# Kernel tuning notes

Hardware: AMD Instinct MI355X
Metric: run time of the kernel (lower is better)

Reference implementation:

```python
import jax, jax.numpy as jnp
import numpy as np

V = 30000      # vocab_size
D = 300        # t_embed
H = 4          # GATv2 heads
C = 300        # per-head out channels (hidden_dim = t_embed)
HID = 768      # hidden_size
B = 2
T = 800
NEG = 0.2      # GATv2 negative_slope default


def gatv2_layer(x, src, dst, Wl, bl, Wr, br, att, bias):
    """PyG GATv2Conv, eval mode, add_self_loops=True, concat=True.
    x: [N, Fin]; src/dst: [E] (src->dst message flow).
    Wl/Wr: [Fin, H*C]; bl/br: [H*C]; att: [H, C]; bias: [H*C].
    """
    N = x.shape[0]
    xl = (x @ Wl + bl).reshape(N, H, C)   # source transform
    xr = (x @ Wr + br).reshape(N, H, C)   # target transform
    loops = jnp.arange(N)
    s = jnp.concatenate([src, loops])
    d = jnp.concatenate([dst, loops])
    e = jax.nn.leaky_relu(xl[s] + xr[d], NEG)          # [E', H, C]
    logits = jnp.einsum('ehc,hc->eh', e, att)           # [E', H]
    # scatter-softmax over incoming edges per target node
    mx = jax.ops.segment_max(logits, d, num_segments=N)  # [N, H]
    ex = jnp.exp(logits - mx[d])
    den = jax.ops.segment_sum(ex, d, num_segments=N)
    alpha = ex / den[d]                                   # [E', H]
    out = jax.ops.segment_sum(alpha[:, :, None] * xl[s], d, num_segments=N)
    return out.reshape(N, H * C) + bias


def setup_inputs() -> dict:
    key = jax.random.key(0)
    ks = jax.random.split(key, 20)
    sc = 0.05
    inp = {
        'kg_enc_input': jax.random.randint(ks[0], (B, T, 3), 0, V),
        'embeddings': jax.random.normal(ks[1], (V, D), jnp.float32),
        # conv1: GATv2Conv(D, C, heads=H)
        'Wl1': jax.random.normal(ks[2], (D, H * C), jnp.float32) * sc,
        'bl1': jnp.zeros((H * C,), jnp.float32),
        'Wr1': jax.random.normal(ks[3], (D, H * C), jnp.float32) * sc,
        'br1': jnp.zeros((H * C,), jnp.float32),
        'att1': jax.random.normal(ks[4], (H, C), jnp.float32) * sc,
        'bias1': jnp.zeros((H * C,), jnp.float32),
        # conv2: GATv2Conv(4*C, C, heads=H)
        'Wl2': jax.random.normal(ks[5], (H * C, H * C), jnp.float32) * sc,
        'bl2': jnp.zeros((H * C,), jnp.float32),
        'Wr2': jax.random.normal(ks[6], (H * C, H * C), jnp.float32) * sc,
        'br2': jnp.zeros((H * C,), jnp.float32),
        'att2': jax.random.normal(ks[7], (H, C), jnp.float32) * sc,
        'bias2': jnp.zeros((H * C,), jnp.float32),
        # post_mp: Linear(4*C, C) -> Dropout -> Linear(C, D)
        'Wp1': jax.random.normal(ks[8], (H * C, C), jnp.float32) * sc,
        'bp1': jnp.zeros((C,), jnp.float32),
        'Wp2': jax.random.normal(ks[9], (C, D), jnp.float32) * sc,
        'bp2': jnp.zeros((D,), jnp.float32),
        # lii: Linear(3*D, HID, bias=False)
        'Wlii': jax.random.normal(ks[10], (3 * D, HID), jnp.float32) * sc,
    }
    return inp


def reference(kg_enc_input, embeddings, Wl1, bl1, Wr1, br1, att1, bias1,
              Wl2, bl2, Wr2, br2, att2, bias2, Wp1, bp1, Wp2, bp2, Wlii):
    # original GAT.forward detaches x -> no grad to embedding table
    x0 = jax.lax.stop_gradient(embeddings)

    def per_sample(kg):  # kg: [T, 3]
        head, rel, tail = kg[:, 0], kg[:, 1], kg[:, 2]
        # edge_list = cat([[head;rel], [rel;tail]], dim=1)
        src = jnp.concatenate([head, rel])
        dst = jnp.concatenate([rel, tail])
        h = gatv2_layer(x0, src, dst, Wl1, bl1, Wr1, br1, att1, bias1)
        h = jax.nn.relu(h)                 # dropout: eval mode, identity
        h = gatv2_layer(h, src, dst, Wl2, bl2, Wr2, br2, att2, bias2)
        h = jax.nn.relu(h)
        w = (h @ Wp1 + bp1) @ Wp2 + bp2    # post_mp, [V, D]
        # per-triple gather + concat of (h, r, t) node embeddings
        return jnp.concatenate([w[head], w[rel], w[tail]], axis=-1)  # [T, 3D]

    final = jax.vmap(per_sample)(kg_enc_input)   # [B, T, 3D]
    return final @ Wlii                           # [B, T, HID]
```

## Files before the change

kernel.cpp:

```cpp
#include <hip/hip_runtime.h>
#include <hip/hip_bf16.h>

#define V 30000
#define D 300
#define H 4
#define C 300
#define HC 1200
#define B 2
#define T 800
#define E 1600
#define MAXM 2400
#define NEG 0.2f
#define SCAN_CH ((MAXM + 255) / 256)

#define MR 2432
#define KD 320
#define KHC 1216
#define NLR 2432
#define WB_LD 304
#define KF 928
#define FRW 896

typedef __attribute__((ext_vector_type(8))) unsigned short u16x8;
typedef __attribute__((ext_vector_type(8))) short s16x8;
typedef __attribute__((ext_vector_type(4))) float f32x4;

__device__ inline unsigned short f2b(float v) {
    unsigned u = __float_as_uint(v);
    unsigned r = (u + 0x7FFFu + ((u >> 16) & 1u)) >> 16;
    return (unsigned short)r;
}
__device__ inline float b2f(unsigned short u) {
    return __uint_as_float(((unsigned)u) << 16);
}

#define GLOAD_LDS16(g, l) __builtin_amdgcn_global_load_lds( \
    (const __attribute__((address_space(1))) void*)(g), \
    (__attribute__((address_space(3))) void*)(l), 16, 0, 0)


__global__ void k_init(int* map, int* list, int* deg, int* fill, int* mcnt) {
    int i = blockIdx.x * blockDim.x + threadIdx.x;
    if (i < B * V) map[i] = -1;
    if (i < B * MAXM) { list[i] = 0; deg[i] = 0; fill[i] = 0; }
    if (i < B) mcnt[i] = 0;
}

__global__ void k_mark(const int* __restrict__ kg, int* map) {
    int i = blockIdx.x * blockDim.x + threadIdx.x;
    if (i >= B * T * 3) return;
    int b = i / (T * 3);
    map[b * V + kg[i]] = 1;
}

__global__ void k_compact(int* map, int* list, int* mcnt) {
    int b = blockIdx.y;
    int i = blockIdx.x * 256 + threadIdx.x;
    bool pred = (i < V) && (map[b * V + i] == 1);
    unsigned long long m = __ballot(pred);
    int lane = threadIdx.x & 63;
    int wid = threadIdx.x >> 6;
    __shared__ int wcnt[4];
    __shared__ int base;
    if (lane == 0) wcnt[wid] = __popcll(m);
    __syncthreads();
    if (threadIdx.x == 0) {
        int t = 0;
#pragma unroll
        for (int w2 = 0; w2 < 4; ++w2) { int c = wcnt[w2]; wcnt[w2] = t; t += c; }
        base = t ? atomicAdd(&mcnt[b], t) : 0;
    }
    __syncthreads();
    if (pred) {
        int idx = base + wcnt[wid] + __popcll(m & ((1ull << lane) - 1ull));
        map[b * V + i] = idx;
        list[b * MAXM + idx] = i;
    }
}

__global__ void k_edges(const int* __restrict__ kg, const int* __restrict__ map,
                        int* esrc, int* edst, int* deg, int* tric) {
    int i = blockIdx.x * blockDim.x + threadIdx.x;
    if (i >= B * T) return;
    int b = i / T, t = i % T;
    const int* kk = kg + ((long)b * T + t) * 3;
    int hc = map[b * V + kk[0]];
    int rc = map[b * V + kk[1]];
    int tc = map[b * V + kk[2]];
    int eb = b * E;
    esrc[eb + t]     = hc;  edst[eb + t]     = rc;
    esrc[eb + T + t] = rc;  edst[eb + T + t] = tc;
    atomicAdd(&deg[b * MAXM + rc], 1);
    atomicAdd(&deg[b * MAXM + tc], 1);
    int* tr = tric + ((long)b * T + t) * 3;
    tr[0] = hc; tr[1] = rc; tr[2] = tc;
}

__global__ void k_scan(const int* __restrict__ deg, int* __restrict__ off) {
    int b = blockIdx.x;
    deg += b * MAXM; off += b * (MAXM + 1);
    __shared__ int ts[256];
    int t = threadIdx.x;
    int base = t * SCAN_CH;
    int loc[SCAN_CH];
    int sum = 0;
#pragma unroll
    for (int j = 0; j < SCAN_CH; ++j) {
        int v = (base + j < MAXM) ? deg[base + j] : 0;
        sum += v; loc[j] = sum;
    }
    ts[t] = sum; __syncthreads();
    for (int s = 1; s < 256; s <<= 1) {
        int v = (t >= s) ? ts[t - s] : 0;
        __syncthreads();
        ts[t] += v;
        __syncthreads();
    }
    int excl = (t > 0) ? ts[t - 1] : 0;
#pragma unroll
    for (int j = 0; j < SCAN_CH; ++j)
        if (base + j < MAXM) off[base + j + 1] = excl + loc[j];
    if (t == 0) off[0] = 0;
}

__global__ void k_scatter(const int* __restrict__ esrc, const int* __restrict__ edst,
                          const int* __restrict__ off, int* fill, int* csr) {
    int i = blockIdx.x * blockDim.x + threadIdx.x;
    if (i >= B * E) return;
    int b = i / E;
    int d = edst[i];
    int pos = off[b * (MAXM + 1) + d] + atomicAdd(&fill[b * MAXM + d], 1);
    csr[b * E + pos] = esrc[i];
}

__global__ void k_wt_all(const float* __restrict__ Wl1, const float* __restrict__ Wr1,
                         const float* __restrict__ Wl2, const float* __restrict__ Wr2,
                         const float* __restrict__ Wp1, const float* __restrict__ Wp2,
                         const float* __restrict__ Wlii,
                         const float* __restrict__ bl1, const float* __restrict__ br1,
                         const float* __restrict__ bl2, const float* __restrict__ br2,
                         unsigned short* Wlr1t, unsigned short* Wlr2t,
                         unsigned short* Wp1t, unsigned short* Wp2t, unsigned short* Wft,
                         float* blr1, float* blr2) {
    const int KT[7]  = {10, 10, 38, 38, 38, 10, 29};
    const int CUM[9] = {0, 380, 760, 2204, 3648, 4104, 4224, 4920, 4930};
    int bid = blockIdx.x;
    int task = 0;
    while (bid >= CUM[task + 1]) ++task;
    int local = bid - CUM[task];
    if (task == 7) {
        int c = local * 256 + threadIdx.y * 32 + threadIdx.x;
        if (c < NLR) {
            float v1 = 0.f, v2 = 0.f;
            if (c < 1200) { v1 = bl1[c]; v2 = bl2[c]; }
            else if (c >= 1216 && c < 2416) { v1 = br1[c - 1216]; v2 = br2[c - 1216]; }
            blr1[c] = v1; blr2[c] = v2;
        }
        return;
    }
    int kt = local % KT[task], nt = local / KT[task];
    const float* W; unsigned short* Wt; int K, N, Kp;
    switch (task) {
        case 0: W = Wl1;  Wt = Wlr1t;                     K = 300;  N = 1200; Kp = KD;  break;
        case 1: W = Wr1;  Wt = Wlr1t + (long)1216 * KD;   K = 300;  N = 1200; Kp = KD;  break;
        case 2: W = Wl2;  Wt = Wlr2t;                     K = 1200; N = 1200; Kp = KHC; break;
        case 3: W = Wr2;  Wt = Wlr2t + (long)1216 * KHC;  K = 1200; N = 1200; Kp = KHC; break;
        case 4: W = Wp1;  Wt = Wp1t;                      K = 1200; N = 300;  Kp = KHC; break;
        case 5: W = Wp2;  Wt = Wp2t;                      K = 300;  N = 300;  Kp = KD;  break;
        default: W = Wlii; Wt = Wft;                      K = 900;  N = 768;  Kp = KF;  break;
    }
    __shared__ float t[32][33];
    int k0 = kt * 32, n0 = nt * 32;
    int tx = threadIdx.x, ty = threadIdx.y;
#pragma unroll
    for (int p = 0; p < 4; ++p) {
        int k = k0 + ty + p * 8, n = n0 + tx;
        t[ty + p * 8][tx] = (k < K && n < N) ? W[(long)k * N + n] : 0.f;
    }
    __syncthreads();
#pragma unroll
    for (int p = 0; p < 4; ++p) {
        int n = n0 + ty + p * 8, k = k0 + tx;
        Wt[(long)n * Kp + k] = f2b(t[tx][ty + p * 8]);
    }
}

__global__ void k_embgather(const float* __restrict__ emb, const int* __restrict__ list,
                            unsigned short* __restrict__ Eb) {
    int b = blockIdx.y, i = blockIdx.x;
    int src = list[b * MAXM + i];
    const float* e = emb + (long)src * D;
    unsigned short* o = Eb + ((long)b * MR + i) * KD;
    int c = threadIdx.x;
    if (c < 75) {
        float4 v = *(const float4*)(e + c * 4);
        ushort4 u;
        u.x = f2b(v.x); u.y = f2b(v.y); u.z = f2b(v.z); u.w = f2b(v.w);
        *(ushort4*)(o + c * 4) = u;
    } else if (c < 80) {
        *(ushort4*)(o + c * 4) = make_ushort4(0, 0, 0, 0);
    }
}

__global__ __launch_bounds__(256) void k_mgemm(
    const unsigned short* __restrict__ A, long sA, int lda,
    const unsigned short* __restrict__ Wt, int ldw,
    const float* __restrict__ bias,
    int M, int N, int K,
    float* __restrict__ outF, long sF, int ldf,
    unsigned short* __restrict__ outB, long sB, int ldb_) {
    int b = blockIdx.z;
    A += (long)b * sA;
    __shared__ unsigned short As[128][32];
    __shared__ unsigned short Bs[128][32];
    int tid = threadIdx.x;

    int nbx = gridDim.x, nby = gridDim.y;
    int nwg = nbx * nby;
    int wg = blockIdx.y * nbx + blockIdx.x;
    int q = nwg >> 3, r8 = nwg & 7;
    int xcd = wg & 7, idx = wg >> 3;
    int L = (xcd < r8 ? xcd * (q + 1) : r8 * (q + 1) + (xcd - r8) * q) + idx;
    const int G = 4;
    int band = L / (G * nbx);
    int first = band * G;
    int sz = min(G, nby - first);
    int rem = L - band * G * nbx;
    int by = first + rem % sz;
    int bx = rem / sz;
    int m0 = by * 128, n0 = bx * 128;

    int w = tid >> 6, lane = tid & 63;
    int wr = (w >> 1) * 64, wc = (w & 1) * 64;
    int fr = lane & 15, fq = lane >> 4;
    int r0 = tid >> 2, sg = tid & 3;
    int swz = (sg ^ ((r0 >> 1) & 3)) * 8;
    const unsigned short* Ap  = A  + (long)(m0 + r0) * lda + swz;
    const unsigned short* Ap2 = A  + (long)(m0 + r0 + 64) * lda + swz;
    const unsigned short* Bp  = Wt + (long)(n0 + r0) * ldw + swz;
    const unsigned short* Bp2 = Wt + (long)(n0 + r0 + 64) * ldw + swz;
    unsigned short* lA  = &As[r0][sg * 8];
    unsigned short* lA2 = &As[r0 + 64][sg * 8];
    unsigned short* lB  = &Bs[r0][sg * 8];
    unsigned short* lB2 = &Bs[r0 + 64][sg * 8];

    f32x4 acc[4][4] = {};
    for (int k0 = 0; k0 < K; k0 += 32) {
        GLOAD_LDS16(Ap + k0, lA);
        GLOAD_LDS16(Ap2 + k0, lA2);
        GLOAD_LDS16(Bp + k0, lB);
        GLOAD_LDS16(Bp2 + k0, lB2);
        __syncthreads();
        s16x8 af[4], bfr[4];
#pragma unroll
        for (int m = 0; m < 4; ++m) {
            int rr = wr + m * 16 + fr;
            af[m] = *(const s16x8*)&As[rr][(fq ^ ((rr >> 1) & 3)) * 8];
        }
#pragma unroll
        for (int n = 0; n < 4; ++n) {
            int rr = wc + n * 16 + fr;
            bfr[n] = *(const s16x8*)&Bs[rr][(fq ^ ((rr >> 1) & 3)) * 8];
        }
#pragma unroll
        for (int m = 0; m < 4; ++m)
#pragma unroll
            for (int n = 0; n < 4; ++n)
                acc[m][n] = __builtin_amdgcn_mfma_f32_16x16x32_bf16(af[m], bfr[n], acc[m][n], 0, 0, 0);
        __syncthreads();
    }
    float* oF = outF ? outF + (long)b * sF : nullptr;
    unsigned short* oB = outB ? outB + (long)b * sB : nullptr;
#pragma unroll
    for (int m = 0; m < 4; ++m) {
        int rb = m0 + wr + m * 16 + fq * 4;
#pragma unroll
        for (int n = 0; n < 4; ++n) {
            int col = n0 + wc + n * 16 + fr;
#pragma unroll
            for (int j = 0; j < 4; ++j) {
                int row = rb + j;
                if (row >= M) continue;
                if (col < N) {
                    float v = acc[m][n][j] + (bias ? bias[col] : 0.f);
                    if (oF) oF[(long)row * ldf + col] = v;
                    if (oB) oB[(long)row * ldb_ + col] = f2b(v);
                } else if (oB && col < ldb_) {
                    oB[(long)row * ldb_ + col] = 0;
                }
            }
        }
    }
}

__global__ __launch_bounds__(256) void k_att(
    const unsigned short* __restrict__ XLR,
    const int* __restrict__ deg, const int* __restrict__ off, const int* __restrict__ csr,
    const float* __restrict__ att, const float* __restrict__ bias,
    unsigned short* __restrict__ OUT) {
    const long sX = (long)MR * NLR;
    const long sO = (long)MR * KHC;
    int b = blockIdx.y;
    int i = blockIdx.x;
    const unsigned short* xl = XLR + (long)b * sX;
    const unsigned short* xr = xl + 1216;
    unsigned short* out = OUT + (long)b * sO;
    int lane = threadIdx.x & 63;
    int h = threadIdx.x >> 6;

    float xr_reg[5], att_reg[5];
#pragma unroll
    for (int q = 0; q < 5; ++q) {
        int c = lane + q * 64;
        if (c < C) {
            xr_reg[q] = b2f(xr[(long)i * NLR + h * C + c]);
            att_reg[q] = att[h * C + c];
        } else { xr_reg[q] = 0.f; att_reg[q] = 0.f; }
    }
    int dg = deg[b * MAXM + i];
    int o0 = off[b * (MAXM + 1) + i];
    const int* cs = csr + b * E;

    float mx = -3e38f, den = 0.f;
    float acc[5] = {0.f, 0.f, 0.f, 0.f, 0.f};
    auto step = [&](int s) {
        const unsigned short* xls = xl + (long)s * NLR + h * C;
        float part = 0.f;
        float xlv[5];
#pragma unroll
        for (int q = 0; q < 5; ++q) {
            int c = lane + q * 64;
            if (c < C) {
                float xv = b2f(xls[c]);
                xlv[q] = xv;
                float v = xv + xr_reg[q];
                v = v > 0.f ? v : NEG * v;
                part += att_reg[q] * v;
            } else xlv[q] = 0.f;
        }
#pragma unroll
        for (int m = 1; m < 64; m <<= 1) part += __shfl_xor(part, m);
        float mn = fmaxf(mx, part);
        float sc = __expf(mx - mn);
        float p = __expf(part - mn);
        den = den * sc + p;
#pragma unroll
        for (int q = 0; q < 5; ++q) acc[q] = acc[q] * sc + p * xlv[q];
        mx = mn;
    };
    step(i);
    for (int e = 0; e < dg; ++e) step(cs[o0 + e]);

    float inv = 1.f / den;
#pragma unroll
    for (int q = 0; q < 5; ++q) {
        int c = lane + q * 64;
        if (c < C) {
            float v = acc[q] * inv + bias[h * C + c];
            out[(long)i * KHC + h * C + c] = f2b(v > 0.f ? v : 0.f);
        }
    }
    if (h == 0 && lane < KHC - HC)
        out[(long)i * KHC + HC + lane] = 0;
}

__global__ void k_fgather(const unsigned short* __restrict__ wb, const int* __restrict__ tric,
                          unsigned short* __restrict__ Af) {
    int b = blockIdx.y, t = blockIdx.x;
    const int* tr = tric + ((long)b * T + t) * 3;
    const unsigned short* w = wb + (long)b * (long)MR * WB_LD;
    unsigned short* o = Af + ((long)b * FRW + t) * KF;
    for (int c = threadIdx.x; c < KF; c += 256) {
        if (c < 900) {
            int part = c / 300, kc = c - part * 300;
            o[c] = w[(long)tr[part] * WB_LD + kc];
        } else o[c] = 0;
    }
}

extern "C" void kernel_launch(void* const* d_in, const int* in_sizes, int n_in,
                              void* d_out, int out_size, void* d_ws, size_t ws_size,
                              hipStream_t stream) {
    const int*   kg    = (const int*)d_in[0];
    const float* emb   = (const float*)d_in[1];
    const float* Wl1   = (const float*)d_in[2];
    const float* bl1   = (const float*)d_in[3];
    const float* Wr1   = (const float*)d_in[4];
    const float* br1   = (const float*)d_in[5];
    const float* att1  = (const float*)d_in[6];
    const float* bias1 = (const float*)d_in[7];
    const float* Wl2   = (const float*)d_in[8];
    const float* bl2   = (const float*)d_in[9];
    const float* Wr2   = (const float*)d_in[10];
    const float* br2   = (const float*)d_in[11];
    const float* att2  = (const float*)d_in[12];
    const float* bias2 = (const float*)d_in[13];
    const float* Wp1   = (const float*)d_in[14];
    const float* bp1   = (const float*)d_in[15];
    const float* Wp2   = (const float*)d_in[16];
    const float* bp2   = (const float*)d_in[17];
    const float* Wlii  = (const float*)d_in[18];
    float* out = (float*)d_out;

    char* ws = (char*)d_ws;
    size_t o = 0;
    auto alloc = [&](size_t bytes) -> void* {
        void* p = ws + o;
        o = (o + bytes + 255) & ~(size_t)255;
        return p;
    };
    int* map  = (int*)alloc(sizeof(int) * B * V);
    int* list = (int*)alloc(sizeof(int) * B * MAXM);
    int* mcnt = (int*)alloc(sizeof(int) * B);
    int* deg  = (int*)alloc(sizeof(int) * B * MAXM);
    int* off  = (int*)alloc(sizeof(int) * B * (MAXM + 1));
    int* fill = (int*)alloc(sizeof(int) * B * MAXM);
    int* esrc = (int*)alloc(sizeof(int) * B * E);
    int* edst = (int*)alloc(sizeof(int) * B * E);
    int* csr  = (int*)alloc(sizeof(int) * B * E);
    int* tric = (int*)alloc(sizeof(int) * B * T * 3);

    long sXlr = (long)MR * NLR;
    long sHb  = (long)MR * KHC;
    long sEb  = (long)MR * KD;
    unsigned short* Xlr = (unsigned short*)alloc(2LL * B * sXlr);
    unsigned short* Hb  = (unsigned short*)alloc(2LL * B * sHb);
    unsigned short* Eb  = (unsigned short*)alloc(2LL * B * sEb);

    unsigned short* Wlr1t = (unsigned short*)alloc(2LL * 2432 * KD);
    unsigned short* Wlr2t = (unsigned short*)alloc(2LL * 2432 * KHC);
    unsigned short* Wp1t  = (unsigned short*)alloc(2LL * 384 * KHC);
    unsigned short* Wp2t  = (unsigned short*)alloc(2LL * 384 * KD);
    unsigned short* Wft   = (unsigned short*)alloc(2LL * 768 * KF);
    float* blr1 = (float*)alloc(sizeof(float) * NLR);
    float* blr2 = (float*)alloc(sizeof(float) * NLR);
    (void)ws_size; (void)in_sizes; (void)n_in; (void)out_size;

    unsigned short* T1b = Eb;
    unsigned short* wb  = Hb;
    unsigned short* Af  = Xlr;

    k_init<<<(B * V + 255) / 256, 256, 0, stream>>>(map, list, deg, fill, mcnt);
    k_mark<<<(B * T * 3 + 255) / 256, 256, 0, stream>>>(kg, map);
    k_compact<<<dim3((V + 255) / 256, B), 256, 0, stream>>>(map, list, mcnt);
    k_edges<<<(B * T + 255) / 256, 256, 0, stream>>>(kg, map, esrc, edst, deg, tric);
    k_scan<<<B, 256, 0, stream>>>(deg, off);
    k_scatter<<<(B * E + 255) / 256, 256, 0, stream>>>(esrc, edst, off, fill, csr);

    k_wt_all<<<4930, dim3(32, 8), 0, stream>>>(Wl1, Wr1, Wl2, Wr2, Wp1, Wp2, Wlii,
                                               bl1, br1, bl2, br2,
                                               Wlr1t, Wlr2t, Wp1t, Wp2t, Wft, blr1, blr2);

    k_embgather<<<dim3(MAXM, B), 128, 0, stream>>>(emb, list, Eb);

    long sWb = (long)MR * WB_LD;
    long sAf = (long)FRW * KF;

    dim3 gL(19, 19, B);
    k_mgemm<<<gL, 256, 0, stream>>>(Eb, sEb, KD, Wlr1t, KD, blr1, MAXM, NLR, KD,
                                    nullptr, 0, 0, Xlr, sXlr, NLR);
    k_att<<<dim3(MAXM, B), 256, 0, stream>>>(Xlr, deg, off, csr, att1, bias1, Hb);
    k_mgemm<<<gL, 256, 0, stream>>>(Hb, sHb, KHC, Wlr2t, KHC, blr2, MAXM, NLR, KHC,
                                    nullptr, 0, 0, Xlr, sXlr, NLR);
    k_att<<<dim3(MAXM, B), 256, 0, stream>>>(Xlr, deg, off, csr, att2, bias2, Hb);
    dim3 gP(3, 19, B);
    k_mgemm<<<gP, 256, 0, stream>>>(Hb, sHb, KHC, Wp1t, KHC, bp1, MAXM, C, KHC,
                                    nullptr, 0, 0, T1b, sEb, KD);
    k_mgemm<<<gP, 256, 0, stream>>>(T1b, sEb, KD, Wp2t, KD, bp2, MAXM, C, KD,
                                    nullptr, 0, 0, wb, sWb, WB_LD);
    k_fgather<<<dim3(T, B), 256, 0, stream>>>(wb, tric, Af);
    k_mgemm<<<dim3(6, 7, B), 256, 0, stream>>>(Af, sAf, KF, Wft, KF, nullptr, T, 768, KF,
                                               out, (long)T * 768, 768, nullptr, 0, 0);
}
```

Before: 349.8 us.

## Fold post_mp weights into one GEMM, fuse triple gather into final GEMM, vectorize attention

The two post_mp linear layers are folded algebraically: Wp1·Wp2 is precomputed once as a small bf16 GEMM on the weights, and the bias bp1·Wp2+bp2 is folded the same way. This replaces the two activation GEMMs with one. The separate triple-gather kernel is removed, and the final GEMM now loads its A tiles straight from the node embedding table using triple indices, with the K dimension padded per part to 320. The attention kernel switches to 4-wide vectorized bf16 loads per lane. The trade-off is an extra small weight GEMM per call and bf16 rounding of the folded weight product.

```diff
diff --git a/kernel.cpp b/kernel.cpp
--- a/kernel.cpp
+++ b/kernel.cpp
@@ -17,8 +17,8 @@
 #define KD 320
 #define KHC 1216
 #define NLR 2432
-#define WB_LD 304
-#define KF 928
+#define WB_LD 320
+#define KF2 960
 #define FRW 896
 
 typedef __attribute__((ext_vector_type(8))) unsigned short u16x8;
@@ -139,17 +139,37 @@
                          const float* __restrict__ Wlii,
                          const float* __restrict__ bl1, const float* __restrict__ br1,
                          const float* __restrict__ bl2, const float* __restrict__ br2,
+                         const float* __restrict__ bp1, const float* __restrict__ bp2,
                          unsigned short* Wlr1t, unsigned short* Wlr2t,
-                         unsigned short* Wp1t, unsigned short* Wp2t, unsigned short* Wft,
-                         float* blr1, float* blr2) {
-    const int KT[7]  = {10, 10, 38, 38, 38, 10, 29};
-    const int CUM[9] = {0, 380, 760, 2204, 3648, 4104, 4224, 4920, 4930};
+                         unsigned short* Wp2t, unsigned short* Wp1b,
+                         unsigned short* Wft2,
+                         float* blr1, float* blr2, float* bp12) {
+    const int KT[6]  = {10, 10, 38, 38, 10, 30};
+    const int CUM[10] = {0, 380, 760, 2204, 3648, 3748, 4468, 4508, 4518, 4520};
     int bid = blockIdx.x;
     int task = 0;
     while (bid >= CUM[task + 1]) ++task;
     int local = bid - CUM[task];
+    int tx = threadIdx.x, ty = threadIdx.y;
+    int tid = ty * 32 + tx;
+
+    if (task == 6) {
+        int r0 = local * 32;
+#pragma unroll
+        for (int p = 0; p < 4; ++p) {
+            int row = r0 + ty + p * 8;
+#pragma unroll
+            for (int j = 0; j < 10; ++j) {
+                int c = tx + j * 32;
+                unsigned short v = 0;
+                if (row < 1200 && c < 300) v = f2b(Wp1[(long)row * 300 + c]);
+                Wp1b[(long)row * 320 + c] = v;
+            }
+        }
+        return;
+    }
     if (task == 7) {
-        int c = local * 256 + threadIdx.y * 32 + threadIdx.x;
+        int c = local * 256 + tid;
         if (c < NLR) {
             float v1 = 0.f, v2 = 0.f;
             if (c < 1200) { v1 = bl1[c]; v2 = bl2[c]; }
@@ -158,6 +178,36 @@
         }
         return;
     }
+    if (task == 8) {
+        int n = local * 256 + tid;
+        if (n < 300) {
+            float s = bp2[n];
+            for (int m = 0; m < 300; ++m) s += bp1[m] * Wp2[(long)m * 300 + n];
+            bp12[n] = s;
+        }
+        return;
+    }
+
+    __shared__ float t[32][33];
+    if (task == 5) {
+        int kt = local % 30, nt = local / 30;
+        int k0 = kt * 32, n0 = nt * 32;
+#pragma unroll
+        for (int p = 0; p < 4; ++p) {
+            int gk = k0 + ty + p * 8, n = n0 + tx;
+            int pp = (gk >= 640) ? 2 : (gk >= 320 ? 1 : 0);
+            int kc = gk - pp * 320;
+            t[ty + p * 8][tx] = (kc < 300) ? Wlii[(long)(300 * pp + kc) * 768 + n] : 0.f;
+        }
+        __syncthreads();
+#pragma unroll
+        for (int p = 0; p < 4; ++p) {
+            int n = n0 + ty + p * 8, gk = k0 + tx;
+            Wft2[(long)n * 960 + gk] = f2b(t[tx][ty + p * 8]);
+        }
+        return;
+    }
+
     int kt = local % KT[task], nt = local / KT[task];
     const float* W; unsigned short* Wt; int K, N, Kp;
     switch (task) {
@@ -165,13 +215,9 @@
         case 1: W = Wr1;  Wt = Wlr1t + (long)1216 * KD;   K = 300;  N = 1200; Kp = KD;  break;
         case 2: W = Wl2;  Wt = Wlr2t;                     K = 1200; N = 1200; Kp = KHC; break;
         case 3: W = Wr2;  Wt = Wlr2t + (long)1216 * KHC;  K = 1200; N = 1200; Kp = KHC; break;
-        case 4: W = Wp1;  Wt = Wp1t;                      K = 1200; N = 300;  Kp = KHC; break;
-        case 5: W = Wp2;  Wt = Wp2t;                      K = 300;  N = 300;  Kp = KD;  break;
-        default: W = Wlii; Wt = Wft;                      K = 900;  N = 768;  Kp = KF;  break;
-    }
-    __shared__ float t[32][33];
+        default: W = Wp2; Wt = Wp2t;                      K = 300;  N = 300;  Kp = KD;  break;
+    }
     int k0 = kt * 32, n0 = nt * 32;
-    int tx = threadIdx.x, ty = threadIdx.y;
 #pragma unroll
     for (int p = 0; p < 4; ++p) {
         int k = k0 + ty + p * 8, n = n0 + tx;
@@ -202,19 +248,7 @@
     }
 }
 
-__global__ __launch_bounds__(256) void k_mgemm(
-    const unsigned short* __restrict__ A, long sA, int lda,
-    const unsigned short* __restrict__ Wt, int ldw,
-    const float* __restrict__ bias,
-    int M, int N, int K,
-    float* __restrict__ outF, long sF, int ldf,
-    unsigned short* __restrict__ outB, long sB, int ldb_) {
-    int b = blockIdx.z;
-    A += (long)b * sA;
-    __shared__ unsigned short As[128][32];
-    __shared__ unsigned short Bs[128][32];
-    int tid = threadIdx.x;
-
+__device__ inline void tile_decode(int& m0, int& n0) {
     int nbx = gridDim.x, nby = gridDim.y;
     int nwg = nbx * nby;
     int wg = blockIdx.y * nbx + blockIdx.x;
@@ -228,7 +262,22 @@
     int rem = L - band * G * nbx;
     int by = first + rem % sz;
     int bx = rem / sz;
-    int m0 = by * 128, n0 = bx * 128;
+    m0 = by * 128; n0 = bx * 128;
+}
+
+__global__ __launch_bounds__(256) void k_mgemm(
+    const unsigned short* __restrict__ A, long sA, int lda,
+    const unsigned short* __restrict__ Wt, int ldw,
+    const float* __restrict__ bias,
+    int M, int N, int K,
+    float* __restrict__ outF, long sF, int ldf,
+    unsigned short* __restrict__ outB, long sB, int ldb_) {
+    int b = blockIdx.z;
+    A += (long)b * sA;
+    __shared__ unsigned short As[128][32];
+    __shared__ unsigned short Bs[128][32];
+    int tid = threadIdx.x;
+    int m0, n0; tile_decode(m0, n0);
 
     int w = tid >> 6, lane = tid & 63;
     int wr = (w >> 1) * 64, wc = (w & 1) * 64;
@@ -288,6 +337,84 @@
                 } else if (oB && col < ldb_) {
                     oB[(long)row * ldb_ + col] = 0;
                 }
+            }
+        }
+    }
+}
+
+__global__ __launch_bounds__(256) void k_fgemm(
+    const unsigned short* __restrict__ wb, long sW,
+    const int* __restrict__ tric,
+    const unsigned short* __restrict__ Wft2,
+    float* __restrict__ out) {
+    int b = blockIdx.z;
+    const unsigned short* wB = wb + (long)b * sW;
+    const int* tr = tric + (long)b * T * 3;
+    float* oF = out + (long)b * T * 768;
+    __shared__ unsigned short As[128][32];
+    __shared__ unsigned short Bs[128][32];
+    int tid = threadIdx.x;
+    int m0, n0; tile_decode(m0, n0);
+
+    int w = tid >> 6, lane = tid & 63;
+    int wr = (w >> 1) * 64, wc = (w & 1) * 64;
+    int fr = lane & 15, fq = lane >> 4;
+    int r0 = tid >> 2, sg = tid & 3;
+    int swz = (sg ^ ((r0 >> 1) & 3)) * 8;
+
+    int gm  = m0 + r0;
+    int gm2 = gm + 64;
+    int t1 = min(gm, T - 1) * 3, t2 = min(gm2, T - 1) * 3;
+    int tr0a = tr[t1], tr1a = tr[t1 + 1], tr2a = tr[t1 + 2];
+    int tr0b = tr[t2], tr1b = tr[t2 + 1], tr2b = tr[t2 + 2];
+
+    const unsigned short* Bp  = Wft2 + (long)(n0 + r0) * KF2 + swz;
+    const unsigned short* Bp2 = Wft2 + (long)(n0 + r0 + 64) * KF2 + swz;
+    unsigned short* lA  = &As[r0][sg * 8];
+    unsigned short* lA2 = &As[r0 + 64][sg * 8];
+    unsigned short* lB  = &Bs[r0][sg * 8];
+    unsigned short* lB2 = &Bs[r0 + 64][sg * 8];
+
+    f32x4 acc[4][4] = {};
+    for (int k0 = 0; k0 < KF2; k0 += 32) {
+        int kk = k0 + swz;
+        int p_ = (kk >= 640) ? 2 : (kk >= 320 ? 1 : 0);
+        int kc = kk - p_ * 320;
+        int tA  = (p_ == 0) ? tr0a : (p_ == 1 ? tr1a : tr2a);
+        int tA2 = (p_ == 0) ? tr0b : (p_ == 1 ? tr1b : tr2b);
+        GLOAD_LDS16(wB + (long)tA * WB_LD + kc, lA);
+        GLOAD_LDS16(wB + (long)tA2 * WB_LD + kc, lA2);
+        GLOAD_LDS16(Bp + k0, lB);
+        GLOAD_LDS16(Bp2 + k0, lB2);
+        __syncthreads();
+        s16x8 af[4], bfr[4];
+#pragma unroll
+        for (int m = 0; m < 4; ++m) {
+            int rr = wr + m * 16 + fr;
+            af[m] = *(const s16x8*)&As[rr][(fq ^ ((rr >> 1) & 3)) * 8];
+        }
+#pragma unroll
+        for (int n = 0; n < 4; ++n) {
+            int rr = wc + n * 16 + fr;
+            bfr[n] = *(const s16x8*)&Bs[rr][(fq ^ ((rr >> 1) & 3)) * 8];
+        }
+#pragma unroll
+        for (int m = 0; m < 4; ++m)
+#pragma unroll
+            for (int n = 0; n < 4; ++n)
+                acc[m][n] = __builtin_amdgcn_mfma_f32_16x16x32_bf16(af[m], bfr[n], acc[m][n], 0, 0, 0);
+        __syncthreads();
+    }
+#pragma unroll
+    for (int m = 0; m < 4; ++m) {
+        int rb = m0 + wr + m * 16 + fq * 4;
+#pragma unroll
+        for (int n = 0; n < 4; ++n) {
+            int col = n0 + wc + n * 16 + fr;
+#pragma unroll
+            for (int j = 0; j < 4; ++j) {
+                int row = rb + j;
+                if (row < T) oF[(long)row * 768 + col] = acc[m][n][j];
             }
         }
     }
@@ -307,36 +434,43 @@
     unsigned short* out = OUT + (long)b * sO;
     int lane = threadIdx.x & 63;
     int h = threadIdx.x >> 6;
-
-    float xr_reg[5], att_reg[5];
-#pragma unroll
-    for (int q = 0; q < 5; ++q) {
-        int c = lane + q * 64;
-        if (c < C) {
-            xr_reg[q] = b2f(xr[(long)i * NLR + h * C + c]);
-            att_reg[q] = att[h * C + c];
-        } else { xr_reg[q] = 0.f; att_reg[q] = 0.f; }
+    int c0 = lane * 4;
+    int c1 = 256 + c0;
+    bool tail = lane < 11;
+
+    float xrf[8], attf[8];
+    {
+        const unsigned short* xp = xr + (long)i * NLR + h * C;
+        ushort4 u0 = *(const ushort4*)(xp + c0);
+        ushort4 u1 = tail ? *(const ushort4*)(xp + c1) : make_ushort4(0, 0, 0, 0);
+        xrf[0] = b2f(u0.x); xrf[1] = b2f(u0.y); xrf[2] = b2f(u0.z); xrf[3] = b2f(u0.w);
+        xrf[4] = b2f(u1.x); xrf[5] = b2f(u1.y); xrf[6] = b2f(u1.z); xrf[7] = b2f(u1.w);
+        float4 a0 = *(const float4*)(att + h * C + c0);
+        attf[0] = a0.x; attf[1] = a0.y; attf[2] = a0.z; attf[3] = a0.w;
+        if (tail) {
+            float4 a1 = *(const float4*)(att + h * C + c1);
+            attf[4] = a1.x; attf[5] = a1.y; attf[6] = a1.z; attf[7] = a1.w;
+        } else { attf[4] = attf[5] = attf[6] = attf[7] = 0.f; }
     }
     int dg = deg[b * MAXM + i];
     int o0 = off[b * (MAXM + 1) + i];
     const int* cs = csr + b * E;
 
     float mx = -3e38f, den = 0.f;
-    float acc[5] = {0.f, 0.f, 0.f, 0.f, 0.f};
+    float acc[8] = {0.f, 0.f, 0.f, 0.f, 0.f, 0.f, 0.f, 0.f};
     auto step = [&](int s) {
-        const unsigned short* xls = xl + (long)s * NLR + h * C;
+        const unsigned short* xp = xl + (long)s * NLR + h * C;
+        ushort4 v0 = *(const ushort4*)(xp + c0);
+        ushort4 v1 = tail ? *(const ushort4*)(xp + c1) : make_ushort4(0, 0, 0, 0);
+        float xv[8];
+        xv[0] = b2f(v0.x); xv[1] = b2f(v0.y); xv[2] = b2f(v0.z); xv[3] = b2f(v0.w);
+        xv[4] = b2f(v1.x); xv[5] = b2f(v1.y); xv[6] = b2f(v1.z); xv[7] = b2f(v1.w);
         float part = 0.f;
-        float xlv[5];
-#pragma unroll
-        for (int q = 0; q < 5; ++q) {
-            int c = lane + q * 64;
-            if (c < C) {
-                float xv = b2f(xls[c]);
-                xlv[q] = xv;
-                float v = xv + xr_reg[q];
-                v = v > 0.f ? v : NEG * v;
-                part += att_reg[q] * v;
-            } else xlv[q] = 0.f;
+#pragma unroll
+        for (int j = 0; j < 8; ++j) {
+            float v = xv[j] + xrf[j];
+            v = v > 0.f ? v : NEG * v;
+            part += attf[j] * v;
         }
 #pragma unroll
         for (int m = 1; m < 64; m <<= 1) part += __shfl_xor(part, m);
@@ -345,37 +479,35 @@
         float p = __expf(part - mn);
         den = den * sc + p;
 #pragma unroll
-        for (int q = 0; q < 5; ++q) acc[q] = acc[q] * sc + p * xlv[q];
+        for (int j = 0; j < 8; ++j) acc[j] = acc[j] * sc + p * xv[j];
         mx = mn;
     };
     step(i);
     for (int e = 0; e < dg; ++e) step(cs[o0 + e]);
 
     float inv = 1.f / den;
-#pragma unroll
-    for (int q = 0; q < 5; ++q) {
-        int c = lane + q * 64;
-        if (c < C) {
-            float v = acc[q] * inv + bias[h * C + c];
-            out[(long)i * KHC + h * C + c] = f2b(v > 0.f ? v : 0.f);
+    unsigned short* op = out + (long)i * KHC + h * C;
+    {
+        float4 b0 = *(const float4*)(bias + h * C + c0);
+        ushort4 s0;
+        float v;
+        v = acc[0] * inv + b0.x; s0.x = f2b(v > 0.f ? v : 0.f);
+        v = acc[1] * inv + b0.y; s0.y = f2b(v > 0.f ? v : 0.f);
+        v = acc[2] * inv + b0.z; s0.z = f2b(v > 0.f ? v : 0.f);
+        v = acc[3] * inv + b0.w; s0.w = f2b(v > 0.f ? v : 0.f);
+        *(ushort4*)(op + c0) = s0;
+        if (tail) {
+            float4 b1 = *(const float4*)(bias + h * C + c1);
+            ushort4 s1;
+            v = acc[4] * inv + b1.x; s1.x = f2b(v > 0.f ? v : 0.f);
+            v = acc[5] * inv + b1.y; s1.y = f2b(v > 0.f ? v : 0.f);
+            v = acc[6] * inv + b1.z; s1.z = f2b(v > 0.f ? v : 0.f);
+            v = acc[7] * inv + b1.w; s1.w = f2b(v > 0.f ? v : 0.f);
+            *(ushort4*)(op + c1) = s1;
         }
     }
     if (h == 0 && lane < KHC - HC)
         out[(long)i * KHC + HC + lane] = 0;
-}
-
-__global__ void k_fgather(const unsigned short* __restrict__ wb, const int* __restrict__ tric,
-                          unsigned short* __restrict__ Af) {
-    int b = blockIdx.y, t = blockIdx.x;
-    const int* tr = tric + ((long)b * T + t) * 3;
-    const unsigned short* w = wb + (long)b * (long)MR * WB_LD;
-    unsigned short* o = Af + ((long)b * FRW + t) * KF;
-    for (int c = threadIdx.x; c < KF; c += 256) {
-        if (c < 900) {
-            int part = c / 300, kc = c - part * 300;
-            o[c] = w[(long)tr[part] * WB_LD + kc];
-        } else o[c] = 0;
-    }
 }
 
 extern "C" void kernel_launch(void* const* d_in, const int* in_sizes, int n_in,
@@ -429,16 +561,16 @@
 
     unsigned short* Wlr1t = (unsigned short*)alloc(2LL * 2432 * KD);
     unsigned short* Wlr2t = (unsigned short*)alloc(2LL * 2432 * KHC);
-    unsigned short* Wp1t  = (unsigned short*)alloc(2LL * 384 * KHC);
     unsigned short* Wp2t  = (unsigned short*)alloc(2LL * 384 * KD);
-    unsigned short* Wft   = (unsigned short*)alloc(2LL * 768 * KF);
+    unsigned short* Wp1b  = (unsigned short*)alloc(2LL * 1280 * 320);
+    unsigned short* Wp12t = (unsigned short*)alloc(2LL * 384 * KHC);
+    unsigned short* Wft2  = (unsigned short*)alloc(2LL * 768 * KF2);
     float* blr1 = (float*)alloc(sizeof(float) * NLR);
     float* blr2 = (float*)alloc(sizeof(float) * NLR);
+    float* bp12 = (float*)alloc(sizeof(float) * 384);
     (void)ws_size; (void)in_sizes; (void)n_in; (void)out_size;
 
-    unsigned short* T1b = Eb;
-    unsigned short* wb  = Hb;
-    unsigned short* Af  = Xlr;
+    unsigned short* wb = Eb;
 
     k_init<<<(B * V + 255) / 256, 256, 0, stream>>>(map, list, deg, fill, mcnt);
     k_mark<<<(B * T * 3 + 255) / 256, 256, 0, stream>>>(kg, map);
@@ -447,14 +579,18 @@
     k_scan<<<B, 256, 0, stream>>>(deg, off);
     k_scatter<<<(B * E + 255) / 256, 256, 0, stream>>>(esrc, edst, off, fill, csr);
 
-    k_wt_all<<<4930, dim3(32, 8), 0, stream>>>(Wl1, Wr1, Wl2, Wr2, Wp1, Wp2, Wlii,
-                                               bl1, br1, bl2, br2,
-                                               Wlr1t, Wlr2t, Wp1t, Wp2t, Wft, blr1, blr2);
+    k_wt_all<<<4520, dim3(32, 8), 0, stream>>>(Wl1, Wr1, Wl2, Wr2, Wp1, Wp2, Wlii,
+                                               bl1, br1, bl2, br2, bp1, bp2,
+                                               Wlr1t, Wlr2t, Wp2t, Wp1b, Wft2,
+                                               blr1, blr2, bp12);
 
     k_embgather<<<dim3(MAXM, B), 128, 0, stream>>>(emb, list, Eb);
 
+    k_mgemm<<<dim3(10, 3, 1), 256, 0, stream>>>(Wp2t, 0, KD, Wp1b, 320, nullptr,
+                                                300, 1216, KD,
+                                                nullptr, 0, 0, Wp12t, 0, KHC);
+
     long sWb = (long)MR * WB_LD;
-    long sAf = (long)FRW * KF;
 
     dim3 gL(19, 19, B);
     k_mgemm<<<gL, 256, 0, stream>>>(Eb, sEb, KD, Wlr1t, KD, blr1, MAXM, NLR, KD,
@@ -463,12 +599,8 @@
     k_mgemm<<<gL, 256, 0, stream>>>(Hb, sHb, KHC, Wlr2t, KHC, blr2, MAXM, NLR, KHC,
                                     nullptr, 0, 0, Xlr, sXlr, NLR);
     k_att<<<dim3(MAXM, B), 256, 0, stream>>>(Xlr, deg, off, csr, att2, bias2, Hb);
-    dim3 gP(3, 19, B);
-    k_mgemm<<<gP, 256, 0, stream>>>(Hb, sHb, KHC, Wp1t, KHC, bp1, MAXM, C, KHC,
-                                    nullptr, 0, 0, T1b, sEb, KD);
-    k_mgemm<<<gP, 256, 0, stream>>>(T1b, sEb, KD, Wp2t, KD, bp2, MAXM, C, KD,
-                                    nullptr, 0, 0, wb, sWb, WB_LD);
-    k_fgather<<<dim3(T, B), 256, 0, stream>>>(wb, tric, Af);
-    k_mgemm<<<dim3(6, 7, B), 256, 0, stream>>>(Af, sAf, KF, Wft, KF, nullptr, T, 768, KF,
-                                               out, (long)T * 768, 768, nullptr, 0, 0);
-}
+    k_mgemm<<<dim3(3, 19, B), 256, 0, stream>>>(Hb, sHb, KHC, Wp12t, KHC, bp12,
+                                                MAXM, 300, KHC,
+                                                nullptr, 0, 0, wb, sWb, WB_LD);
+    k_fgemm<<<dim3(6, 7, B), 256, 0, stream>>>(wb, sWb, tric, Wft2, out);
+}
```

After: 346.4 us. No clear change (-1.0%).
